# Kernel tuning notes

Hardware: AMD Instinct MI355X
Metric: run time of the kernel (lower is better)

The kernel has to match this reference:

```python
import jax, jax.numpy as jnp
import numpy as np

D_MODEL = 1024
D_INNER = 2048
D_STATE = 16
DT_RANK = 64
D_CONV = 4
B = 1
L = 2048


def setup_inputs() -> dict:
    key = jax.random.key(0)
    ks = jax.random.split(key, 8)
    s = 0.02
    x = jax.random.normal(ks[0], (B, L, D_MODEL), dtype=jnp.float32)
    in_w = jax.random.normal(ks[1], (D_MODEL, 2 * D_INNER), dtype=jnp.float32) * s
    conv_w = jax.random.normal(ks[2], (D_INNER, 1, D_CONV), dtype=jnp.float32) * s
    conv_b = jnp.zeros((D_INNER,), dtype=jnp.float32)
    x_proj_w = jax.random.normal(ks[3], (D_INNER, DT_RANK + 2 * D_STATE), dtype=jnp.float32) * s
    dt_w = jax.random.normal(ks[4], (DT_RANK, D_INNER), dtype=jnp.float32) * s
    dt_b = jax.random.normal(ks[5], (D_INNER,), dtype=jnp.float32) * s
    A_log = jnp.log(jnp.broadcast_to(jnp.arange(1, D_STATE + 1, dtype=jnp.float32), (D_INNER, D_STATE)))
    D = jnp.ones((D_INNER,), dtype=jnp.float32)
    out_w = jax.random.normal(ks[6], (D_INNER, D_MODEL), dtype=jnp.float32) * s
    norm_w = jnp.ones((D_MODEL,), dtype=jnp.float32)
    return dict(x=x, in_w=in_w, conv_w=conv_w, conv_b=conv_b, x_proj_w=x_proj_w,
                dt_w=dt_w, dt_b=dt_b, A_log=A_log, D=D, out_w=out_w, norm_w=norm_w)


def _forward(x, in_w, conv_w, conv_b, x_proj_w, dt_w, dt_b, A_log, D, out_w, norm_w):
    eps = 1e-5
    # RMSNorm
    h = x * jax.lax.rsqrt(jnp.mean(x * x, axis=-1, keepdims=True) + eps) * norm_w
    # in_proj -> split into conv path u and gate res
    xr = h @ in_w  # [b, l, 2*d_inner]
    u, res = jnp.split(xr, 2, axis=-1)
    # causal depthwise conv1d (left pad d_conv-1, truncate to l)
    ut = jnp.transpose(u, (0, 2, 1))  # [b, d_inner, l]
    conv = jax.lax.conv_general_dilated(
        ut, conv_w, window_strides=(1,), padding=((D_CONV - 1, 0),),
        feature_group_count=D_INNER, dimension_numbers=('NCH', 'OIH', 'NCH'))
    conv = conv + conv_b[None, :, None]
    u = jax.nn.silu(jnp.transpose(conv, (0, 2, 1)))  # [b, l, d_inner]
    # SSM parameterization
    x_dbl = u @ x_proj_w  # [b, l, dt_rank + 2*d_state]
    dt, Bm, Cm = jnp.split(x_dbl, [DT_RANK, DT_RANK + D_STATE], axis=-1)
    delta = jax.nn.softplus(dt @ dt_w + dt_b)  # [b, l, d_inner]
    A = -jnp.exp(A_log)  # [d_inner, d_state]
    dA = jnp.exp(jnp.einsum('bld,dn->bldn', delta, A))        # [b, l, d_inner, d_state]
    dBu = jnp.einsum('bld,bln->bldn', delta * u, Bm)           # [b, l, d_inner, d_state]
    # sequential selective scan over l via lax.scan
    def step(s, inp):
        dA_t, dBu_t, C_t = inp
        s = dA_t * s + dBu_t                     # [b, d_inner, d_state]
        y = jnp.einsum('bdn,bn->bd', s, C_t)     # [b, d_inner]
        return s, y
    s0 = jnp.zeros((x.shape[0], D_INNER, D_STATE), dtype=jnp.float32)
    _, ys = jax.lax.scan(step, s0, (jnp.transpose(dA, (1, 0, 2, 3)),
                                    jnp.transpose(dBu, (1, 0, 2, 3)),
                                    jnp.transpose(Cm, (1, 0, 2))))
    y = jnp.transpose(ys, (1, 0, 2)) + u * D  # [b, l, d_inner]
    # gated output + residual
    y = y * jax.nn.silu(res)
    return y @ out_w + x


def reference(x, in_w, conv_w, conv_b, x_proj_w, dt_w, dt_b, A_log, D, out_w, norm_w):
    return _forward(x, in_w, conv_w, conv_b, x_proj_w, dt_w, dt_b, A_log, D, out_w, norm_w)
```

## Files before the change

### kernel.cpp

```cpp
#include <hip/hip_runtime.h>
#include <hip/hip_bf16.h>
#include <math.h>

#define LSEQ   2048
#define DMODEL 1024
#define DINNER 2048
#define DSTATE 16
#define DTRANK 64
#define NCH    64
#define TCH    32
#define KSPLIT 16

typedef __hip_bfloat16 bf16;
typedef __attribute__((ext_vector_type(8))) short short8;
typedef __attribute__((ext_vector_type(4))) float f32x4;

#define MB (1024u*1024u)
#define OFFB_HBF   (0u)
#define OFFB_INWT  (4u*MB)
#define OFFB_OUTWT (12u*MB)
#define OFFB_YGBF  (16u*MB)
#define OFFB_XR    (24u*MB)
#define OFFB_UC    (56u*MB)
#define OFFB_XDBL  (72u*MB)
#define OFFB_DELTA (73u*MB)
#define OFFB_SLOC  (89u*MB)
#define OFFB_DSUM  (97u*MB)
#define OFFB_SINIT (98u*MB)
#define OFFB_DTBF  (106u*MB)
#define OFFB_DTWT  (107u*MB)
#define OFFB_XPART OFFB_SLOC

static __device__ __forceinline__ unsigned short f2bf_u16(float f) {
    bf16 b = __float2bfloat16(f);
    return *reinterpret_cast<unsigned short*>(&b);
}

static __device__ __forceinline__ void async_copy16(const void* g, void* l) {
    __builtin_amdgcn_global_load_lds(
        (const __attribute__((address_space(1))) unsigned int*)g,
        (__attribute__((address_space(3))) unsigned int*)l, 16, 0, 0);
}

__global__ __launch_bounds__(256) void rmsnorm_k(
    const float* __restrict__ x, const float* __restrict__ nw,
    unsigned short* __restrict__ hb)
{
    int t = blockIdx.x;
    const float4* xp = (const float4*)(x + t * DMODEL);
    float4 v = xp[threadIdx.x];
    float ss = v.x*v.x + v.y*v.y + v.z*v.z + v.w*v.w;
    #pragma unroll
    for (int o = 32; o > 0; o >>= 1) ss += __shfl_down(ss, o);
    __shared__ float red[4];
    int lane = threadIdx.x & 63, wid = threadIdx.x >> 6;
    if (lane == 0) red[wid] = ss;
    __syncthreads();
    float tot = red[0] + red[1] + red[2] + red[3];
    float sc = rsqrtf(tot / (float)DMODEL + 1e-5f);
    float4 w4 = ((const float4*)nw)[threadIdx.x];
    ushort4 o4;
    o4.x = f2bf_u16(v.x * sc * w4.x);
    o4.y = f2bf_u16(v.y * sc * w4.y);
    o4.z = f2bf_u16(v.z * sc * w4.z);
    o4.w = f2bf_u16(v.w * sc * w4.w);
    ((ushort4*)(hb + t * DMODEL))[threadIdx.x] = o4;
}

__global__ __launch_bounds__(256) void transpose_bf16_k(
    const float* __restrict__ W, unsigned short* __restrict__ WT, int R, int C)
{
    __shared__ float tile[32][33];
    int c0 = blockIdx.x * 32;
    int r0 = blockIdx.y * 32;
    int tx = threadIdx.x & 31;
    int ty = threadIdx.x >> 5;
    #pragma unroll
    for (int i = 0; i < 4; i++) {
        int r = ty + i*8;
        tile[r][tx] = W[(long)(r0 + r)*C + c0 + tx];
    }
    __syncthreads();
    #pragma unroll
    for (int i = 0; i < 4; i++) {
        int c = ty + i*8;
        WT[(long)(c0 + c)*R + r0 + tx] = f2bf_u16(tile[tx][c]);
    }
}

template<int NT, int EPI>
__global__ __launch_bounds__(256) void gemm_mfma_k(
    const unsigned short* __restrict__ A, const unsigned short* __restrict__ BT,
    float* __restrict__ C, const float* __restrict__ addv,
    int M, int N, int K)
{
    constexpr int NI = NT / 32;
    __shared__ short As[128 * 32];
    __shared__ short Bs[NT * 32];
    int tid = threadIdx.x;
    int lane = tid & 63;
    int w = tid >> 6;
    int m0 = blockIdx.y * 128;
    int n0 = blockIdx.x * NT;
    int wm = (w & 1) * 64;
    int wn = (w >> 1) * (NT / 2);

    f32x4 acc[4][NI];
    #pragma unroll
    for (int i = 0; i < 4; i++)
        #pragma unroll
        for (int j = 0; j < NI; j++) acc[i][j] = (f32x4){0.f,0.f,0.f,0.f};

    int mrow = lane & 15;
    int kq   = lane >> 4;

    for (int k0 = 0; k0 < K; k0 += 32) {
        __syncthreads();
        #pragma unroll
        for (int j = 0; j < 2; j++) {
            int i = j*256 + tid;
            int row = i >> 2;
            int kb = (i & 3) * 8;
            async_copy16(A + (long)(m0 + row)*K + k0 + kb,
                         (char*)As + (((j*256 + (w<<6)) << 4)));
        }
        #pragma unroll
        for (int j = 0; j < NT/64; j++) {
            int i = j*256 + tid;
            int row = i >> 2;
            int kb = (i & 3) * 8;
            async_copy16(BT + (long)(n0 + row)*K + k0 + kb,
                         (char*)Bs + (((j*256 + (w<<6)) << 4)));
        }
        __syncthreads();
        short8 af[4], bf[NI];
        #pragma unroll
        for (int mi = 0; mi < 4; mi++)
            af[mi] = *(const short8*)&As[(wm + mi*16 + mrow)*32 + kq*8];
        #pragma unroll
        for (int ni = 0; ni < NI; ni++)
            bf[ni] = *(const short8*)&Bs[(wn + ni*16 + mrow)*32 + kq*8];
        #pragma unroll
        for (int mi = 0; mi < 4; mi++)
            #pragma unroll
            for (int ni = 0; ni < NI; ni++)
                acc[mi][ni] = __builtin_amdgcn_mfma_f32_16x16x32_bf16(
                    af[mi], bf[ni], acc[mi][ni], 0, 0, 0);
    }

    int cn = lane & 15;
    int cr = (lane >> 4) * 4;
    #pragma unroll
    for (int mi = 0; mi < 4; mi++) {
        #pragma unroll
        for (int ni = 0; ni < NI; ni++) {
            #pragma unroll
            for (int r = 0; r < 4; r++) {
                long row = m0 + wm + mi*16 + cr + r;
                long col = n0 + wn + ni*16 + cn;
                long idx = row * N + col;
                float v = acc[mi][ni][r];
                if (EPI == 1) v += addv[idx];
                if (EPI == 2) {
                    v += addv[col];
                    v = (v > 20.f) ? v : log1pf(__expf(v));
                }
                C[idx] = v;
            }
        }
    }
}

__global__ __launch_bounds__(256) void conv_silu_k(
    const float* __restrict__ xr, const float* __restrict__ cw,
    const float* __restrict__ cb, float* __restrict__ uc)
{
    int idx = blockIdx.x * 256 + threadIdx.x;
    int t = idx >> 11;
    int d = idx & (DINNER - 1);
    float4 w = *(const float4*)(cw + d * 4);
    float acc = cb[d];
    if (t >= 3) acc += xr[(t-3)*4096 + d] * w.x;
    if (t >= 2) acc += xr[(t-2)*4096 + d] * w.y;
    if (t >= 1) acc += xr[(t-1)*4096 + d] * w.z;
    acc += xr[t*4096 + d] * w.w;
    uc[idx] = acc / (1.f + __expf(-acc));
}

__global__ __launch_bounds__(256) void xproj_part_k(
    const float* __restrict__ uc, const float* __restrict__ xw,
    float* __restrict__ xpart)
{
    __shared__ float Us[32][68];
    __shared__ float Ws[32][96];
    int tid = threadIdx.x;
    int kc = blockIdx.x;
    int m0 = blockIdx.y * 64;
    int kbase = kc * (DINNER / KSPLIT);
    int tx = tid & 31;
    int ty = tid >> 5;
    float acc[8][3];
    #pragma unroll
    for (int i = 0; i < 8; i++)
        #pragma unroll
        for (int c = 0; c < 3; c++) acc[i][c] = 0.f;

    int ur = tid >> 2;
    int ukq = (tid & 3) * 8;
    int wk = tid >> 3;
    int wc = (tid & 7) * 12;

    for (int kb = 0; kb < DINNER / KSPLIT; kb += 32) {
        int k1 = kbase + kb;
        __syncthreads();
        float4 a0 = *(const float4*)(uc + (long)(m0 + ur)*DINNER + k1 + ukq);
        float4 a1 = *(const float4*)(uc + (long)(m0 + ur)*DINNER + k1 + ukq + 4);
        Us[ukq+0][ur] = a0.x; Us[ukq+1][ur] = a0.y;
        Us[ukq+2][ur] = a0.z; Us[ukq+3][ur] = a0.w;
        Us[ukq+4][ur] = a1.x; Us[ukq+5][ur] = a1.y;
        Us[ukq+6][ur] = a1.z; Us[ukq+7][ur] = a1.w;
        #pragma unroll
        for (int j = 0; j < 3; j++)
            *(float4*)&Ws[wk][wc + 4*j] =
                *(const float4*)(xw + (long)(k1 + wk)*96 + wc + 4*j);
        __syncthreads();
        #pragma unroll
        for (int k = 0; k < 32; k++) {
            float4 u0 = *(const float4*)&Us[k][ty*8];
            float4 u1 = *(const float4*)&Us[k][ty*8 + 4];
            float w0 = Ws[k][tx*3 + 0];
            float w1 = Ws[k][tx*3 + 1];
            float w2 = Ws[k][tx*3 + 2];
            float uu[8] = {u0.x,u0.y,u0.z,u0.w, u1.x,u1.y,u1.z,u1.w};
            #pragma unroll
            for (int i = 0; i < 8; i++) {
                acc[i][0] += uu[i]*w0;
                acc[i][1] += uu[i]*w1;
                acc[i][2] += uu[i]*w2;
            }
        }
    }
    float* dst = xpart + (long)kc * LSEQ * 96;
    #pragma unroll
    for (int i = 0; i < 8; i++) {
        long row = m0 + ty*8 + i;
        #pragma unroll
        for (int c = 0; c < 3; c++)
            dst[row*96 + tx*3 + c] = acc[i][c];
    }
}

__global__ __launch_bounds__(256) void xproj_reduce_k(
    const float* __restrict__ xpart, float* __restrict__ xdbl,
    unsigned short* __restrict__ dtbf)
{
    int idx = blockIdx.x * 256 + threadIdx.x;
    int i4 = idx * 4;
    float4 s = *(const float4*)(xpart + i4);
    #pragma unroll
    for (int p = 1; p < KSPLIT; p++) {
        float4 v = *(const float4*)(xpart + (long)p * LSEQ * 96 + i4);
        s.x += v.x; s.y += v.y; s.z += v.z; s.w += v.w;
    }
    *(float4*)(xdbl + i4) = s;
    int row = idx / 24;
    int col = (idx % 24) * 4;
    if (col < DTRANK) {
        ushort4 o;
        o.x = f2bf_u16(s.x); o.y = f2bf_u16(s.y);
        o.z = f2bf_u16(s.z); o.w = f2bf_u16(s.w);
        *(ushort4*)(dtbf + row * DTRANK + col) = o;
    }
}

__global__ __launch_bounds__(256) void scanA_k(
    const float* __restrict__ delta, const float* __restrict__ uc,
    const float* __restrict__ xdbl, const float* __restrict__ alog,
    float* __restrict__ sloc, float* __restrict__ dsum)
{
    int c  = blockIdx.x >> 3;
    int dg = blockIdx.x & 7;
    int d  = dg * 256 + threadIdx.x;
    float a[16];
    #pragma unroll
    for (int n = 0; n < 16; n++) a[n] = -__expf(alog[d*16 + n]);
    float s[16];
    #pragma unroll
    for (int n = 0; n < 16; n++) s[n] = 0.f;
    float ds = 0.f;
    int t0 = c * TCH;
    for (int t = t0; t < t0 + TCH; t++) {
        float dl = delta[t*DINNER + d];
        float uu = uc[t*DINNER + d];
        float du = dl * uu;
        ds += dl;
        const float4* bp = (const float4*)(xdbl + t*96 + DTRANK);
        float4 b0 = bp[0], b1 = bp[1], b2 = bp[2], b3 = bp[3];
        float bv[16] = {b0.x,b0.y,b0.z,b0.w, b1.x,b1.y,b1.z,b1.w,
                        b2.x,b2.y,b2.z,b2.w, b3.x,b3.y,b3.z,b3.w};
        #pragma unroll
        for (int n = 0; n < 16; n++)
            s[n] = __expf(a[n]*dl) * s[n] + du * bv[n];
    }
    #pragma unroll
    for (int n = 0; n < 16; n++)
        sloc[(c*16 + n)*DINNER + d] = s[n];
    dsum[c*DINNER + d] = ds;
}

__global__ __launch_bounds__(256) void scanB_k(
    const float* __restrict__ alog, const float* __restrict__ dsum,
    const float* __restrict__ sloc, float* __restrict__ sinit)
{
    int i = blockIdx.x * 256 + threadIdx.x;
    int d = i & (DINNER - 1);
    int n = i >> 11;
    float a = -__expf(alog[d*16 + n]);
    float s = 0.f;
    for (int c = 0; c < NCH; c++) {
        int idx = (c*16 + n)*DINNER + d;
        sinit[idx] = s;
        s = __expf(a * dsum[c*DINNER + d]) * s + sloc[idx];
    }
}

__global__ __launch_bounds__(256) void scanC_k(
    const float* __restrict__ delta, const float* __restrict__ uc,
    const float* __restrict__ xdbl, const float* __restrict__ alog,
    const float* __restrict__ sinit, const float* __restrict__ Dv,
    const float* __restrict__ xr, unsigned short* __restrict__ ygb)
{
    int c  = blockIdx.x >> 3;
    int dg = blockIdx.x & 7;
    int d  = dg * 256 + threadIdx.x;
    float a[16];
    #pragma unroll
    for (int n = 0; n < 16; n++) a[n] = -__expf(alog[d*16 + n]);
    float s[16];
    #pragma unroll
    for (int n = 0; n < 16; n++) s[n] = sinit[(c*16 + n)*DINNER + d];
    float dvv = Dv[d];
    int t0 = c * TCH;
    for (int t = t0; t < t0 + TCH; t++) {
        float dl = delta[t*DINNER + d];
        float uu = uc[t*DINNER + d];
        float du = dl * uu;
        const float4* bp = (const float4*)(xdbl + t*96 + DTRANK);
        float4 b0 = bp[0], b1 = bp[1], b2 = bp[2], b3 = bp[3];
        const float4* cp = (const float4*)(xdbl + t*96 + DTRANK + DSTATE);
        float4 c0 = cp[0], c1 = cp[1], c2 = cp[2], c3 = cp[3];
        float bv[16] = {b0.x,b0.y,b0.z,b0.w, b1.x,b1.y,b1.z,b1.w,
                        b2.x,b2.y,b2.z,b2.w, b3.x,b3.y,b3.z,b3.w};
        float cv[16] = {c0.x,c0.y,c0.z,c0.w, c1.x,c1.y,c1.z,c1.w,
                        c2.x,c2.y,c2.z,c2.w, c3.x,c3.y,c3.z,c3.w};
        float y = 0.f;
        #pragma unroll
        for (int n = 0; n < 16; n++) {
            s[n] = __expf(a[n]*dl) * s[n] + du * bv[n];
            y += s[n] * cv[n];
        }
        y += uu * dvv;
        float r = xr[t*4096 + DINNER + d];
        ygb[t*DINNER + d] = f2bf_u16(y * (r / (1.f + __expf(-r))));
    }
}

extern "C" void kernel_launch(void* const* d_in, const int* in_sizes, int n_in,
                              void* d_out, int out_size, void* d_ws, size_t ws_size,
                              hipStream_t stream)
{
    const float* x      = (const float*)d_in[0];
    const float* in_w   = (const float*)d_in[1];
    const float* conv_w = (const float*)d_in[2];
    const float* conv_b = (const float*)d_in[3];
    const float* xpw    = (const float*)d_in[4];
    const float* dtw    = (const float*)d_in[5];
    const float* dtb    = (const float*)d_in[6];
    const float* alog   = (const float*)d_in[7];
    const float* Dv     = (const float*)d_in[8];
    const float* outw   = (const float*)d_in[9];
    const float* normw  = (const float*)d_in[10];

    char* wsb = (char*)d_ws;
    unsigned short* hb    = (unsigned short*)(wsb + OFFB_HBF);
    unsigned short* inwt  = (unsigned short*)(wsb + OFFB_INWT);
    unsigned short* outwt = (unsigned short*)(wsb + OFFB_OUTWT);
    unsigned short* ygb   = (unsigned short*)(wsb + OFFB_YGBF);
    unsigned short* dtbf  = (unsigned short*)(wsb + OFFB_DTBF);
    unsigned short* dtwt  = (unsigned short*)(wsb + OFFB_DTWT);
    float* xr    = (float*)(wsb + OFFB_XR);
    float* uc    = (float*)(wsb + OFFB_UC);
    float* xdbl  = (float*)(wsb + OFFB_XDBL);
    float* delta = (float*)(wsb + OFFB_DELTA);
    float* sloc  = (float*)(wsb + OFFB_SLOC);
    float* dsum  = (float*)(wsb + OFFB_DSUM);
    float* sinit = (float*)(wsb + OFFB_SINIT);
    float* xpart = (float*)(wsb + OFFB_XPART);
    float* out   = (float*)d_out;

    hipLaunchKernelGGL(transpose_bf16_k, dim3(4096/32, 1024/32), dim3(256), 0, stream,
                       in_w, inwt, DMODEL, 2*DINNER);
    hipLaunchKernelGGL(transpose_bf16_k, dim3(1024/32, 2048/32), dim3(256), 0, stream,
                       outw, outwt, DINNER, DMODEL);
    hipLaunchKernelGGL(transpose_bf16_k, dim3(2048/32, 64/32), dim3(256), 0, stream,
                       dtw, dtwt, DTRANK, DINNER);

    hipLaunchKernelGGL(rmsnorm_k, dim3(LSEQ), dim3(256), 0, stream, x, normw, hb);
    hipLaunchKernelGGL((gemm_mfma_k<128,0>), dim3(4096/128, 2048/128), dim3(256), 0,
                       stream, hb, inwt, xr, (const float*)nullptr, LSEQ, 2*DINNER, DMODEL);
    hipLaunchKernelGGL(conv_silu_k, dim3(LSEQ*DINNER/256), dim3(256), 0, stream,
                       xr, conv_w, conv_b, uc);
    hipLaunchKernelGGL(xproj_part_k, dim3(KSPLIT, LSEQ/64), dim3(256), 0, stream,
                       uc, xpw, xpart);
    hipLaunchKernelGGL(xproj_reduce_k, dim3(LSEQ*96/4/256), dim3(256), 0, stream,
                       xpart, xdbl, dtbf);
    hipLaunchKernelGGL((gemm_mfma_k<128,2>), dim3(2048/128, 2048/128), dim3(256), 0,
                       stream, dtbf, dtwt, delta, dtb, LSEQ, DINNER, DTRANK);
    hipLaunchKernelGGL(scanA_k, dim3(NCH*8), dim3(256), 0, stream,
                       delta, uc, xdbl, alog, sloc, dsum);
    hipLaunchKernelGGL(scanB_k, dim3(128), dim3(256), 0, stream, alog, dsum, sloc, sinit);
    hipLaunchKernelGGL(scanC_k, dim3(NCH*8), dim3(256), 0, stream,
                       delta, uc, xdbl, alog, sinit, Dv, xr, ygb);
    hipLaunchKernelGGL((gemm_mfma_k<64,1>), dim3(1024/64, 2048/128), dim3(256), 0,
                       stream, ygb, outwt, out, x, LSEQ, DMODEL, DINNER);
}
```

Measured before the change: 288.0 us.

## Store in_proj output as bf16 and split-K the out_proj GEMM

The in_proj GEMM now writes its 2048x4096 result as bf16 instead of fp32. This halves the bytes written there and read back by the conv and gating stages, at the cost of some precision in u and the gate. The out_proj GEMM is split into 4 K-slices that write fp32 partials into the freed xr region. A new reduce kernel sums the partials and adds the residual. The split raises the out_proj grid from 256 to 1024 blocks to fill more CUs, but adds partial-buffer traffic and one more launch.

```diff
diff --git a/kernel.cpp b/kernel.cpp
--- a/kernel.cpp
+++ b/kernel.cpp
@@ -10,6 +10,7 @@
 #define NCH    64
 #define TCH    32
 #define KSPLIT 16
+#define KS2    4
 
 typedef __hip_bfloat16 bf16;
 typedef __attribute__((ext_vector_type(8))) short short8;
@@ -30,10 +31,14 @@
 #define OFFB_DTBF  (106u*MB)
 #define OFFB_DTWT  (107u*MB)
 #define OFFB_XPART OFFB_SLOC
+#define OFFB_OPART OFFB_XR
 
 static __device__ __forceinline__ unsigned short f2bf_u16(float f) {
     bf16 b = __float2bfloat16(f);
     return *reinterpret_cast<unsigned short*>(&b);
+}
+static __device__ __forceinline__ float bfu16_f(unsigned short u) {
+    union { float f; unsigned int i; } v; v.i = ((unsigned int)u) << 16; return v.f;
 }
 
 static __device__ __forceinline__ void async_copy16(const void* g, void* l) {
@@ -91,8 +96,8 @@
 template<int NT, int EPI>
 __global__ __launch_bounds__(256) void gemm_mfma_k(
     const unsigned short* __restrict__ A, const unsigned short* __restrict__ BT,
-    float* __restrict__ C, const float* __restrict__ addv,
-    int M, int N, int K)
+    void* __restrict__ Cv, const float* __restrict__ addv,
+    int M, int N, int K, int lda, int ldb)
 {
     constexpr int NI = NT / 32;
     __shared__ short As[128 * 32];
@@ -104,6 +109,7 @@
     int n0 = blockIdx.x * NT;
     int wm = (w & 1) * 64;
     int wn = (w >> 1) * (NT / 2);
+    long koff = (long)blockIdx.z * K;
 
     f32x4 acc[4][NI];
     #pragma unroll
@@ -121,7 +127,7 @@
             int i = j*256 + tid;
             int row = i >> 2;
             int kb = (i & 3) * 8;
-            async_copy16(A + (long)(m0 + row)*K + k0 + kb,
+            async_copy16(A + (long)(m0 + row)*lda + koff + k0 + kb,
                          (char*)As + (((j*256 + (w<<6)) << 4)));
         }
         #pragma unroll
@@ -129,7 +135,7 @@
             int i = j*256 + tid;
             int row = i >> 2;
             int kb = (i & 3) * 8;
-            async_copy16(BT + (long)(n0 + row)*K + k0 + kb,
+            async_copy16(BT + (long)(n0 + row)*ldb + koff + k0 + kb,
                          (char*)Bs + (((j*256 + (w<<6)) << 4)));
         }
         __syncthreads();
@@ -150,6 +156,8 @@
 
     int cn = lane & 15;
     int cr = (lane >> 4) * 4;
+    float* Cf = (float*)Cv + (long)blockIdx.z * M * N;
+    unsigned short* Cb = (unsigned short*)Cv;
     #pragma unroll
     for (int mi = 0; mi < 4; mi++) {
         #pragma unroll
@@ -160,19 +168,33 @@
                 long col = n0 + wn + ni*16 + cn;
                 long idx = row * N + col;
                 float v = acc[mi][ni][r];
-                if (EPI == 1) v += addv[idx];
                 if (EPI == 2) {
                     v += addv[col];
                     v = (v > 20.f) ? v : log1pf(__expf(v));
                 }
-                C[idx] = v;
+                if (EPI == 3) Cb[idx] = f2bf_u16(v);
+                else          Cf[idx] = v;
             }
         }
     }
 }
 
+__global__ __launch_bounds__(256) void out_reduce_k(
+    const float* __restrict__ opart, const float* __restrict__ x,
+    float* __restrict__ out)
+{
+    int i4 = (blockIdx.x * 256 + threadIdx.x) * 4;
+    float4 s = *(const float4*)(x + i4);
+    #pragma unroll
+    for (int z = 0; z < KS2; z++) {
+        float4 v = *(const float4*)(opart + (long)z * LSEQ * DMODEL + i4);
+        s.x += v.x; s.y += v.y; s.z += v.z; s.w += v.w;
+    }
+    *(float4*)(out + i4) = s;
+}
+
 __global__ __launch_bounds__(256) void conv_silu_k(
-    const float* __restrict__ xr, const float* __restrict__ cw,
+    const unsigned short* __restrict__ xrb, const float* __restrict__ cw,
     const float* __restrict__ cb, float* __restrict__ uc)
 {
     int idx = blockIdx.x * 256 + threadIdx.x;
@@ -180,10 +202,10 @@
     int d = idx & (DINNER - 1);
     float4 w = *(const float4*)(cw + d * 4);
     float acc = cb[d];
-    if (t >= 3) acc += xr[(t-3)*4096 + d] * w.x;
-    if (t >= 2) acc += xr[(t-2)*4096 + d] * w.y;
-    if (t >= 1) acc += xr[(t-1)*4096 + d] * w.z;
-    acc += xr[t*4096 + d] * w.w;
+    if (t >= 3) acc += bfu16_f(xrb[(t-3)*4096 + d]) * w.x;
+    if (t >= 2) acc += bfu16_f(xrb[(t-2)*4096 + d]) * w.y;
+    if (t >= 1) acc += bfu16_f(xrb[(t-1)*4096 + d]) * w.z;
+    acc += bfu16_f(xrb[t*4096 + d]) * w.w;
     uc[idx] = acc / (1.f + __expf(-acc));
 }
 
@@ -328,7 +350,7 @@
     const float* __restrict__ delta, const float* __restrict__ uc,
     const float* __restrict__ xdbl, const float* __restrict__ alog,
     const float* __restrict__ sinit, const float* __restrict__ Dv,
-    const float* __restrict__ xr, unsigned short* __restrict__ ygb)
+    const unsigned short* __restrict__ xrb, unsigned short* __restrict__ ygb)
 {
     int c  = blockIdx.x >> 3;
     int dg = blockIdx.x & 7;
@@ -360,7 +382,7 @@
             y += s[n] * cv[n];
         }
         y += uu * dvv;
-        float r = xr[t*4096 + DINNER + d];
+        float r = bfu16_f(xrb[t*4096 + DINNER + d]);
         ygb[t*DINNER + d] = f2bf_u16(y * (r / (1.f + __expf(-r))));
     }
 }
@@ -388,7 +410,7 @@
     unsigned short* ygb   = (unsigned short*)(wsb + OFFB_YGBF);
     unsigned short* dtbf  = (unsigned short*)(wsb + OFFB_DTBF);
     unsigned short* dtwt  = (unsigned short*)(wsb + OFFB_DTWT);
-    float* xr    = (float*)(wsb + OFFB_XR);
+    unsigned short* xrb   = (unsigned short*)(wsb + OFFB_XR);
     float* uc    = (float*)(wsb + OFFB_UC);
     float* xdbl  = (float*)(wsb + OFFB_XDBL);
     float* delta = (float*)(wsb + OFFB_DELTA);
@@ -396,6 +418,7 @@
     float* dsum  = (float*)(wsb + OFFB_DSUM);
     float* sinit = (float*)(wsb + OFFB_SINIT);
     float* xpart = (float*)(wsb + OFFB_XPART);
+    float* opart = (float*)(wsb + OFFB_OPART);
     float* out   = (float*)d_out;
 
     hipLaunchKernelGGL(transpose_bf16_k, dim3(4096/32, 1024/32), dim3(256), 0, stream,
@@ -406,21 +429,26 @@
                        dtw, dtwt, DTRANK, DINNER);
 
     hipLaunchKernelGGL(rmsnorm_k, dim3(LSEQ), dim3(256), 0, stream, x, normw, hb);
-    hipLaunchKernelGGL((gemm_mfma_k<128,0>), dim3(4096/128, 2048/128), dim3(256), 0,
-                       stream, hb, inwt, xr, (const float*)nullptr, LSEQ, 2*DINNER, DMODEL);
+    hipLaunchKernelGGL((gemm_mfma_k<128,3>), dim3(4096/128, 2048/128, 1), dim3(256), 0,
+                       stream, hb, inwt, (void*)xrb, (const float*)nullptr,
+                       LSEQ, 2*DINNER, DMODEL, DMODEL, DMODEL);
     hipLaunchKernelGGL(conv_silu_k, dim3(LSEQ*DINNER/256), dim3(256), 0, stream,
-                       xr, conv_w, conv_b, uc);
+                       xrb, conv_w, conv_b, uc);
     hipLaunchKernelGGL(xproj_part_k, dim3(KSPLIT, LSEQ/64), dim3(256), 0, stream,
                        uc, xpw, xpart);
     hipLaunchKernelGGL(xproj_reduce_k, dim3(LSEQ*96/4/256), dim3(256), 0, stream,
                        xpart, xdbl, dtbf);
-    hipLaunchKernelGGL((gemm_mfma_k<128,2>), dim3(2048/128, 2048/128), dim3(256), 0,
-                       stream, dtbf, dtwt, delta, dtb, LSEQ, DINNER, DTRANK);
+    hipLaunchKernelGGL((gemm_mfma_k<128,2>), dim3(2048/128, 2048/128, 1), dim3(256), 0,
+                       stream, dtbf, dtwt, (void*)delta, dtb,
+                       LSEQ, DINNER, DTRANK, DTRANK, DTRANK);
     hipLaunchKernelGGL(scanA_k, dim3(NCH*8), dim3(256), 0, stream,
                        delta, uc, xdbl, alog, sloc, dsum);
     hipLaunchKernelGGL(scanB_k, dim3(128), dim3(256), 0, stream, alog, dsum, sloc, sinit);
     hipLaunchKernelGGL(scanC_k, dim3(NCH*8), dim3(256), 0, stream,
-                       delta, uc, xdbl, alog, sinit, Dv, xr, ygb);
-    hipLaunchKernelGGL((gemm_mfma_k<64,1>), dim3(1024/64, 2048/128), dim3(256), 0,
-                       stream, ygb, outwt, out, x, LSEQ, DMODEL, DINNER);
-}
+                       delta, uc, xdbl, alog, sinit, Dv, xrb, ygb);
+    hipLaunchKernelGGL((gemm_mfma_k<64,0>), dim3(1024/64, 2048/128, KS2), dim3(256), 0,
+                       stream, ygb, outwt, (void*)opart, (const float*)nullptr,
+                       LSEQ, DMODEL, DINNER/KS2, DINNER, DINNER);
+    hipLaunchKernelGGL(out_reduce_k, dim3(LSEQ*DMODEL/4/256), dim3(256), 0, stream,
+                       opart, x, out);
+}
```

After: 277.1 us. 1.04x faster.
